# Kernel optimization log

Hardware: AMD Instinct MI355X
Metric: run time of the kernel (lower is better)

## Reference

```python
import jax, jax.numpy as jnp
import numpy as np

B, N, C = 2, 32768, 512
L, H = 64, 8
DH = C // H
NB = N // L
EG_HID = 16


def setup_inputs() -> dict:
    key = jax.random.key(0)
    ks = jax.random.split(key, 12)
    x = jax.random.normal(ks[0], (B, N, C), dtype=jnp.float32)
    attn_mask = jax.random.randint(ks[1], (NB, L, L), 0, 2, dtype=jnp.int32)
    edge_feats = jax.random.normal(ks[2], (NB, L, L, 4), dtype=jnp.float32)
    s = 1.0 / np.sqrt(C)
    w_qkv = jax.random.normal(ks[3], (C, 3 * C), dtype=jnp.float32) * s
    b_qkv = jnp.zeros((3 * C,), dtype=jnp.float32)
    w_proj = jax.random.normal(ks[4], (C, C), dtype=jnp.float32) * s
    b_proj = jnp.zeros((C,), dtype=jnp.float32)
    w_eg1 = jax.random.normal(ks[5], (4, EG_HID), dtype=jnp.float32) * 0.01
    b_eg1 = jnp.zeros((EG_HID,), dtype=jnp.float32)
    w_eg2 = jax.random.normal(ks[6], (EG_HID, H), dtype=jnp.float32) * 0.01
    b_eg2 = jnp.zeros((H,), dtype=jnp.float32)
    w_blk = jax.random.normal(ks[7], (C, H), dtype=jnp.float32) * 0.01
    b_blk = jnp.zeros((H,), dtype=jnp.float32)
    return {"x": x, "attn_mask": attn_mask, "edge_feats": edge_feats,
            "w_qkv": w_qkv, "b_qkv": b_qkv, "w_proj": w_proj, "b_proj": b_proj,
            "w_eg1": w_eg1, "b_eg1": b_eg1, "w_eg2": w_eg2, "b_eg2": b_eg2,
            "w_blk": w_blk, "b_blk": b_blk}


def reference(x, attn_mask, edge_feats, w_qkv, b_qkv, w_proj, b_proj,
              w_eg1, b_eg1, w_eg2, b_eg2, w_blk, b_blk):
    scale = DH ** -0.5
    x_blk = x.reshape(B, NB, L, C)
    # bias_physics: (B, NB, L, L, 4), expanded across batch
    bias = jnp.broadcast_to(edge_feats[None], (B, NB, L, L, 4))
    idx = jnp.arange(L)
    # zero diagonal, set channel 3 of diagonal to 1
    bias = bias.at[:, :, idx, idx, :].set(0.0)
    bias = bias.at[:, :, idx, idx, 3].set(1.0)
    # mask: (B, NB, L, L); ensure each query row attends to at least itself
    mask = jnp.broadcast_to(attn_mask[None], (B, NB, L, L))
    need_diag = (mask.sum(axis=-1) < 1).astype(mask.dtype)  # (B, NB, L)
    diag = mask[:, :, idx, idx]
    mask = mask.at[:, :, idx, idx].set(jnp.maximum(diag, need_diag))
    # qkv
    qkv = x_blk @ w_qkv + b_qkv  # (B, NB, L, 3C)
    q = qkv[..., :C].reshape(B, NB, L, H, DH)
    k = qkv[..., C:2 * C].reshape(B, NB, L, H, DH)
    v = qkv[..., 2 * C:].reshape(B, NB, L, H, DH)
    scores = jnp.einsum('bnqhd,bnkhd->bnqkh', q, k) * scale
    scores = scores + bias[..., 3:4]
    mask_e = (mask[..., None] == 0)  # (B, NB, L, L, 1)
    scores = jnp.where(mask_e, -jnp.inf, scores)
    attn_probs = jax.nn.softmax(scores, axis=3)
    # edge-gate MLP: 4 -> 16 (exact GELU) -> H
    gate = jax.nn.gelu(bias @ w_eg1 + b_eg1, approximate=False) @ w_eg2 + b_eg2
    gate = jnp.where(mask_e, 0.0, gate)
    combined = attn_probs + gate
    x_mid = jnp.einsum('bnqkh,bnkhd->bnqhd', combined, v)  # (B, NB, L, H, DH)
    # block route token
    block_node = x_blk.mean(axis=2, keepdims=True)  # (B, NB, 1, C)
    v_block = (block_node @ w_qkv + b_qkv)[..., 2 * C:].reshape(B, NB, 1, H, DH)
    g_block = jax.nn.sigmoid(x_blk @ w_blk + b_blk)  # (B, NB, L, H)
    x_mid = x_mid + g_block[..., None] * v_block
    out = x_mid.reshape(B, NB, L, C) @ w_proj + b_proj
    return out.reshape(B, N, C)
```

## Files before the change

kernel.cpp:

```cpp
#include <hip/hip_runtime.h>

typedef unsigned short u16;
typedef __attribute__((ext_vector_type(8))) short bf16x8;
typedef __attribute__((ext_vector_type(4))) float f32x4;

#define NTOK 32768
#define CC 512
#define HH 8
#define LL 64
#define NBLK 512

__device__ __forceinline__ u16 f2bf(float f) {
    unsigned int u = __float_as_uint(f);
    unsigned int r = u + 0x7fffu + ((u >> 16) & 1u);
    return (u16)(r >> 16);
}
__device__ __forceinline__ float bf2f(u16 h) {
    return __uint_as_float(((unsigned int)h) << 16);
}
__device__ __forceinline__ bf16x8 bc8(uint4 v) {
    return __builtin_bit_cast(bf16x8, v);
}
__device__ __forceinline__ void dma16(const u16* g, u16* l) {
    __builtin_amdgcn_global_load_lds((const __attribute__((address_space(1))) void*)g,
                                     (__attribute__((address_space(3))) void*)l, 16, 0, 0);
}

__global__ __launch_bounds__(256) void convert_gblock_kernel(const float* __restrict__ x,
                                                             u16* __restrict__ xbf,
                                                             const float* __restrict__ w_blk,
                                                             const float* __restrict__ b_blk,
                                                             float* __restrict__ gbl) {
    __shared__ float wbs[4608];
    int tid = threadIdx.x;
    for (int i = tid; i < 4096; i += 256) wbs[i + (i >> 6)] = w_blk[i];
    size_t tok = (size_t)blockIdx.x * 4 + (tid >> 6);
    int lane = tid & 63;
    int c0 = lane * 8;
    const float4* p = (const float4*)(x + tok * CC + c0);
    float4 a = p[0], b = p[1];
    uint4 o;
    o.x = (unsigned)f2bf(a.x) | ((unsigned)f2bf(a.y) << 16);
    o.y = (unsigned)f2bf(a.z) | ((unsigned)f2bf(a.w) << 16);
    o.z = (unsigned)f2bf(b.x) | ((unsigned)f2bf(b.y) << 16);
    o.w = (unsigned)f2bf(b.z) | ((unsigned)f2bf(b.w) << 16);
    *(uint4*)(xbf + tok * CC + c0) = o;
    float xv[8] = {a.x, a.y, a.z, a.w, b.x, b.y, b.z, b.w};
    __syncthreads();
    float acc[8];
#pragma unroll
    for (int h = 0; h < 8; ++h) acc[h] = 0.f;
#pragma unroll
    for (int j = 0; j < 8; ++j) {
        const float* wr = &wbs[(c0 + j) * 8 + lane];
#pragma unroll
        for (int h = 0; h < 8; ++h) acc[h] += xv[j] * wr[h];
    }
#pragma unroll
    for (int h = 0; h < 8; ++h) {
#pragma unroll
        for (int off = 1; off < 64; off <<= 1) acc[h] += __shfl_xor(acc[h], off);
    }
    float v = acc[0];
#pragma unroll
    for (int h = 1; h < 8; ++h) v = (lane == h) ? acc[h] : v;
    if (lane < 8) gbl[tok * 8 + lane] = 1.f / (1.f + __expf(-(v + b_blk[lane])));
}

__global__ __launch_bounds__(256) void transpose_bf16_kernel(const float* __restrict__ in,
                                                             u16* __restrict__ out,
                                                             int K, int Nn) {
    __shared__ float tile[32][33];
    int n0 = blockIdx.x * 32, k0 = blockIdx.y * 32;
    int tx = threadIdx.x & 31, ty = threadIdx.x >> 5;
#pragma unroll
    for (int i = 0; i < 4; ++i)
        tile[ty + i * 8][tx] = in[(size_t)(k0 + ty + i * 8) * Nn + n0 + tx];
    __syncthreads();
#pragma unroll
    for (int i = 0; i < 4; ++i)
        out[(size_t)(n0 + ty + i * 8) * K + k0 + tx] = f2bf(tile[tx][ty + i * 8]);
}

__global__ __launch_bounds__(256) void gate_sbias_kernel(const int* __restrict__ mask,
                                                         const float* __restrict__ edge,
                                                         const float* __restrict__ w1,
                                                         const float* __restrict__ b1,
                                                         const float* __restrict__ w2,
                                                         const float* __restrict__ b2,
                                                         u16* __restrict__ gate2,
                                                         u16* __restrict__ sbias2) {
    __shared__ float w1s[64], b1s[16], w2s[128], b2s[8];
    __shared__ int nds[64];
    int t = threadIdx.x;
    int nb = blockIdx.x;
    if (t < 64) w1s[t] = w1[t];
    if (t < 16) b1s[t] = b1[t];
    if (t < 128) w2s[t] = w2[t];
    if (t < 8) b2s[t] = b2[t];
    if (t < 64) {
        int s = 0;
        const int* mr = mask + (size_t)(nb * 64 + t) * 64;
#pragma unroll 8
        for (int k = 0; k < 64; ++k) s += mr[k];
        nds[t] = (s < 1) ? 1 : 0;
    }
    __syncthreads();
#pragma unroll 1
    for (int it = 0; it < 16; ++it) {
        int p = it * 256 + t;
        int q = p >> 6, k = p & 63;
        int pk = (k & 15) * 4 + (k >> 4);
        int mv = mask[(size_t)(nb * 64 + q) * 64 + k];
        float e0, e1, e2, e3;
        if (q == k) {
            mv = max(mv, nds[q]);
            e0 = e1 = e2 = 0.f;
            e3 = 1.f;
        } else {
            const float* ep = edge + ((size_t)(nb * 64 + q) * 64 + k) * 4;
            e0 = ep[0]; e1 = ep[1]; e2 = ep[2]; e3 = ep[3];
        }
        sbias2[(size_t)(nb * 64 + q) * 64 + pk] = f2bf(mv ? e3 : -1e30f);
        float g[8];
#pragma unroll
        for (int hh = 0; hh < 8; ++hh) g[hh] = b2s[hh];
#pragma unroll
        for (int j = 0; j < 16; ++j) {
            float hpre = e0 * w1s[j] + e1 * w1s[16 + j] + e2 * w1s[32 + j] + e3 * w1s[48 + j] + b1s[j];
            float hg = 0.5f * hpre * (1.f + erff(hpre * 0.70710678f));
#pragma unroll
            for (int hh = 0; hh < 8; ++hh) g[hh] += hg * w2s[j * 8 + hh];
        }
#pragma unroll
        for (int hh = 0; hh < 8; ++hh)
            gate2[(((size_t)nb * 8 + hh) * 64 + q) * 64 + pk] = f2bf(mv ? g[hh] : 0.f);
    }
}

__global__ __launch_bounds__(256) void qkv_gemm_kernel(const u16* __restrict__ xbf,
                                                       const u16* __restrict__ wqkvT,
                                                       const float* __restrict__ b_qkv,
                                                       u16* __restrict__ qkv) {
    __shared__ __align__(16) u16 As[128 * 64], Bs[128 * 64];
    int tid = threadIdx.x;
    int n0 = blockIdx.x * 128;
    int m0 = blockIdx.y * 128;
    int lane = tid & 63, l15 = lane & 15, quad = lane >> 4, wave = tid >> 6;
    int r8 = lane >> 3, jch = lane & 7;
    int js = jch ^ r8;
    int mwl = (wave >> 1) * 64, nwl = (wave & 1) * 64;
    int sw = l15 & 7;

    f32x4 acc[4][4];
#pragma unroll
    for (int i = 0; i < 4; ++i)
#pragma unroll
        for (int j = 0; j < 4; ++j) acc[i][j] = (f32x4){0.f, 0.f, 0.f, 0.f};

    int arow[4], brow[4];
#pragma unroll
    for (int i = 0; i < 4; ++i) arow[i] = (mwl + i * 16 + l15) * 64;
#pragma unroll
    for (int j = 0; j < 4; ++j) brow[j] = (nwl + j * 16 + l15) * 64;

    const u16* gA = xbf + (size_t)(m0 + wave * 32 + r8) * CC + js * 8;
    const u16* gB = wqkvT + (size_t)(n0 + wave * 32 + r8) * CC + js * 8;
    u16* lA = As + wave * 32 * 64;
    u16* lB = Bs + wave * 32 * 64;

    for (int kt = 0; kt < 8; ++kt) {
        int k0 = kt * 64;
#pragma unroll
        for (int t = 0; t < 4; ++t) {
            dma16(gA + (size_t)t * 8 * CC + k0, lA + t * 8 * 64);
            dma16(gB + (size_t)t * 8 * CC + k0, lB + t * 8 * 64);
        }
        __syncthreads();
#pragma unroll
        for (int kk = 0; kk < 2; ++kk) {
            int ch = ((kk * 4 + quad) ^ sw) * 8;
            bf16x8 a[4], bb[4];
#pragma unroll
            for (int i = 0; i < 4; ++i) a[i] = *(const bf16x8*)&As[arow[i] + ch];
#pragma unroll
            for (int j = 0; j < 4; ++j) bb[j] = *(const bf16x8*)&Bs[brow[j] + ch];
#pragma unroll
            for (int i = 0; i < 4; ++i)
#pragma unroll
                for (int j = 0; j < 4; ++j)
                    acc[i][j] = __builtin_amdgcn_mfma_f32_16x16x32_bf16(a[i], bb[j], acc[i][j], 0, 0, 0);
        }
        __syncthreads();
    }
#pragma unroll
    for (int i = 0; i < 4; ++i)
#pragma unroll
        for (int j = 0; j < 4; ++j) {
            int col = n0 + nwl + j * 16 + l15;
            float bp = b_qkv[col];
#pragma unroll
            for (int r = 0; r < 4; ++r) {
                int row = m0 + mwl + i * 16 + quad * 4 + r;
                qkv[(size_t)row * 1536 + col] = f2bf(acc[i][j][r] + bp);
            }
        }
}

__global__ __launch_bounds__(256) void outproj_kernel(const u16* __restrict__ xmid,
                                                      const u16* __restrict__ wprojT,
                                                      const float* __restrict__ b_proj,
                                                      float* __restrict__ out) {
    __shared__ __align__(16) u16 As[128 * 64], Bs[128 * 64];
    int tid = threadIdx.x;
    int n0 = blockIdx.x * 128;
    int m0 = blockIdx.y * 128;
    int lane = tid & 63, l15 = lane & 15, quad = lane >> 4, wave = tid >> 6;
    int r8 = lane >> 3, jch = lane & 7;
    int js = jch ^ r8;
    int mwl = (wave >> 1) * 64, nwl = (wave & 1) * 64;
    int sw = l15 & 7;

    f32x4 acc[4][4];
#pragma unroll
    for (int i = 0; i < 4; ++i)
#pragma unroll
        for (int j = 0; j < 4; ++j) acc[i][j] = (f32x4){0.f, 0.f, 0.f, 0.f};

    int arow[4], brow[4];
#pragma unroll
    for (int i = 0; i < 4; ++i) arow[i] = (mwl + i * 16 + l15) * 64;
#pragma unroll
    for (int j = 0; j < 4; ++j) brow[j] = (nwl + j * 16 + l15) * 64;

    const u16* gA = xmid + (size_t)(m0 + wave * 32 + r8) * CC + js * 8;
    const u16* gB = wprojT + (size_t)(n0 + wave * 32 + r8) * CC + js * 8;
    u16* lA = As + wave * 32 * 64;
    u16* lB = Bs + wave * 32 * 64;

    for (int kt = 0; kt < 8; ++kt) {
        int k0 = kt * 64;
#pragma unroll
        for (int t = 0; t < 4; ++t) {
            dma16(gA + (size_t)t * 8 * CC + k0, lA + t * 8 * 64);
            dma16(gB + (size_t)t * 8 * CC + k0, lB + t * 8 * 64);
        }
        __syncthreads();
#pragma unroll
        for (int kk = 0; kk < 2; ++kk) {
            int ch = ((kk * 4 + quad) ^ sw) * 8;
            bf16x8 a[4], bb[4];
#pragma unroll
            for (int i = 0; i < 4; ++i) a[i] = *(const bf16x8*)&As[arow[i] + ch];
#pragma unroll
            for (int j = 0; j < 4; ++j) bb[j] = *(const bf16x8*)&Bs[brow[j] + ch];
#pragma unroll
            for (int i = 0; i < 4; ++i)
#pragma unroll
                for (int j = 0; j < 4; ++j)
                    acc[i][j] = __builtin_amdgcn_mfma_f32_16x16x32_bf16(a[i], bb[j], acc[i][j], 0, 0, 0);
        }
        __syncthreads();
    }
#pragma unroll
    for (int i = 0; i < 4; ++i)
#pragma unroll
        for (int j = 0; j < 4; ++j) {
            int col = n0 + nwl + j * 16 + l15;
            float bp = b_proj[col];
#pragma unroll
            for (int r = 0; r < 4; ++r) {
                int row = m0 + mwl + i * 16 + quad * 4 + r;
                out[(size_t)row * CC + col] = acc[i][j][r] + bp;
            }
        }
}

__global__ __launch_bounds__(256) void attn_kernel(const u16* __restrict__ qkv,
                                                   const u16* __restrict__ sbias2,
                                                   const u16* __restrict__ gate2,
                                                   const float* __restrict__ gbl,
                                                   u16* __restrict__ xmid) {
    __shared__ u16 VT[64 * 72], Ps[64 * 72];
    __shared__ float gl[64], vbl[64];
    int tid = threadIdx.x;
    int bid = blockIdx.x;
    int h = bid & 7, nb = (bid >> 3) & 511, b = bid >> 12;
    int lane = tid & 63, l15 = lane & 15, quad = lane >> 4, wave = tid >> 6;
    int m0 = wave * 16;
    size_t blockrow = (size_t)(b * NTOK + nb * 64);
    const u16* qbase = qkv + blockrow * 1536 + h * 64;

    {
        int key = tid & 63, d0 = (tid >> 6) * 16;
        const uint4* vsrc = (const uint4*)(qbase + (size_t)key * 1536 + 1024 + d0);
        uint4 v0 = vsrc[0], v1 = vsrc[1];
        u16 tmp[16];
        *(uint4*)tmp = v0;
        *(uint4*)(tmp + 8) = v1;
#pragma unroll
        for (int j = 0; j < 16; ++j) VT[(d0 + j) * 72 + key] = tmp[j];
    }
    if (tid < 64) gl[tid] = gbl[(blockrow + tid) * 8 + h];
    __syncthreads();

    if (tid < 64) {
        float s = 0.f;
#pragma unroll 8
        for (int k = 0; k < 64; ++k) s += bf2f(VT[tid * 72 + k]);
        vbl[tid] = s * 0.015625f;
    }

    f32x4 sc[4];
#pragma unroll
    for (int t = 0; t < 4; ++t) sc[t] = (f32x4){0.f, 0.f, 0.f, 0.f};
#pragma unroll
    for (int kk = 0; kk < 2; ++kk) {
        bf16x8 a = bc8(*(const uint4*)(qbase + (size_t)(m0 + l15) * 1536 + kk * 32 + quad * 8));
#pragma unroll
        for (int t = 0; t < 4; ++t) {
            bf16x8 bb = bc8(*(const uint4*)(qbase + (size_t)(t * 16 + l15) * 1536 + 512 + kk * 32 + quad * 8));
            sc[t] = __builtin_amdgcn_mfma_f32_16x16x32_bf16(a, bb, sc[t], 0, 0, 0);
        }
    }
    {
        const u16* sb2 = sbias2 + (size_t)nb * 4096;
        const u16* gp2 = gate2 + ((size_t)nb * 8 + h) * 4096;
#pragma unroll
        for (int r = 0; r < 4; ++r) {
            int q = m0 + quad * 4 + r;
            ushort4 sv = *(const ushort4*)(sb2 + (q * 16 + l15) * 4);
            float bias_t[4] = {bf2f(sv.x), bf2f(sv.y), bf2f(sv.z), bf2f(sv.w)};
            float mx = -3e38f;
#pragma unroll
            for (int t = 0; t < 4; ++t) {
                float v = sc[t][r] * 0.125f + bias_t[t];
                sc[t][r] = v;
                mx = fmaxf(mx, v);
            }
            mx = fmaxf(mx, __shfl_xor(mx, 1));
            mx = fmaxf(mx, __shfl_xor(mx, 2));
            mx = fmaxf(mx, __shfl_xor(mx, 4));
            mx = fmaxf(mx, __shfl_xor(mx, 8));
            float sum = 0.f;
#pragma unroll
            for (int t = 0; t < 4; ++t) {
                float p = __expf(sc[t][r] - mx);
                sc[t][r] = p;
                sum += p;
            }
            sum += __shfl_xor(sum, 1);
            sum += __shfl_xor(sum, 2);
            sum += __shfl_xor(sum, 4);
            sum += __shfl_xor(sum, 8);
            float inv = 1.f / sum;
            ushort4 gv = *(const ushort4*)(gp2 + (q * 16 + l15) * 4);
            float gate_t[4] = {bf2f(gv.x), bf2f(gv.y), bf2f(gv.z), bf2f(gv.w)};
#pragma unroll
            for (int t = 0; t < 4; ++t) {
                float comb = sc[t][r] * inv + gate_t[t];
                Ps[q * 72 + t * 16 + l15] = f2bf(comb);
            }
        }
    }
    __syncthreads();

    f32x4 o[4];
#pragma unroll
    for (int t = 0; t < 4; ++t) o[t] = (f32x4){0.f, 0.f, 0.f, 0.f};
#pragma unroll
    for (int kk = 0; kk < 2; ++kk) {
        bf16x8 a = *(const bf16x8*)&Ps[(m0 + l15) * 72 + kk * 32 + quad * 8];
#pragma unroll
        for (int t = 0; t < 4; ++t) {
            bf16x8 bb = *(const bf16x8*)&VT[(t * 16 + l15) * 72 + kk * 32 + quad * 8];
            o[t] = __builtin_amdgcn_mfma_f32_16x16x32_bf16(a, bb, o[t], 0, 0, 0);
        }
    }
#pragma unroll
    for (int t = 0; t < 4; ++t) {
#pragma unroll
        for (int r = 0; r < 4; ++r) {
            int q = m0 + quad * 4 + r, d = t * 16 + l15;
            float v = o[t][r] + gl[q] * vbl[d];
            xmid[(blockrow + q) * CC + h * 64 + d] = f2bf(v);
        }
    }
}

extern "C" void kernel_launch(void* const* d_in, const int* in_sizes, int n_in,
                              void* d_out, int out_size, void* d_ws, size_t ws_size,
                              hipStream_t stream) {
    const float* x = (const float*)d_in[0];
    const int* attn_mask = (const int*)d_in[1];
    const float* edge = (const float*)d_in[2];
    const float* w_qkv = (const float*)d_in[3];
    const float* b_qkv = (const float*)d_in[4];
    const float* w_proj = (const float*)d_in[5];
    const float* b_proj = (const float*)d_in[6];
    const float* w_eg1 = (const float*)d_in[7];
    const float* b_eg1 = (const float*)d_in[8];
    const float* w_eg2 = (const float*)d_in[9];
    const float* b_eg2 = (const float*)d_in[10];
    const float* w_blk = (const float*)d_in[11];
    const float* b_blk = (const float*)d_in[12];
    float* out = (float*)d_out;

    char* ws = (char*)d_ws;
    u16* xbf = (u16*)ws;
    u16* xmid = (u16*)ws;
    u16* qkv = (u16*)(ws + 67108864);
    u16* gate2 = (u16*)(ws + 268435456);
    u16* sbias2 = (u16*)(ws + 301989888);
    u16* wqkvT = (u16*)(ws + 306184192);
    u16* wprojT = (u16*)(ws + 307757056);
    float* gbl = (float*)(ws + 308281344);

    convert_gblock_kernel<<<16384, 256, 0, stream>>>(x, xbf, w_blk, b_blk, gbl);
    transpose_bf16_kernel<<<dim3(48, 16), 256, 0, stream>>>(w_qkv, wqkvT, 512, 1536);
    transpose_bf16_kernel<<<dim3(16, 16), 256, 0, stream>>>(w_proj, wprojT, 512, 512);
    gate_sbias_kernel<<<512, 256, 0, stream>>>(attn_mask, edge, w_eg1, b_eg1, w_eg2, b_eg2,
                                               gate2, sbias2);
    qkv_gemm_kernel<<<dim3(12, 512), 256, 0, stream>>>(xbf, wqkvT, b_qkv, qkv);
    attn_kernel<<<8192, 256, 0, stream>>>(qkv, sbias2, gate2, gbl, xmid);
    outproj_kernel<<<dim3(4, 512), 256, 0, stream>>>(xmid, wprojT, b_proj, out);
}
```

Before: 718.0 us.

## Store QKV head-planar, remap GEMM blocks per XCD, split gate kernel

The QKV GEMM now writes its output in a head-planar layout (plane of 64 columns × all tokens), so the attention kernel reads contiguous 128-byte rows for Q, K and V instead of rows strided by 1536 elements. Both GEMMs use a flat 1D grid with a block-index remap that groups consecutive logical tiles onto the same XCD (stride 8), to improve L2 reuse of the A and B tiles. The gate/sbias kernel is split four ways over query rows to raise parallelism. The planar store scatters writes at 64-element granularity, which may cost some write efficiency in the GEMM epilogue.

```diff
diff --git a/kernel.cpp b/kernel.cpp
--- a/kernel.cpp
+++ b/kernel.cpp
@@ -9,6 +9,7 @@
 #define HH 8
 #define LL 64
 #define NBLK 512
+#define MTOK 65536
 
 __device__ __forceinline__ u16 f2bf(float f) {
     unsigned int u = __float_as_uint(f);
@@ -91,30 +92,33 @@
                                                          u16* __restrict__ gate2,
                                                          u16* __restrict__ sbias2) {
     __shared__ float w1s[64], b1s[16], w2s[128], b2s[8];
-    __shared__ int nds[64];
+    __shared__ int nds[16];
     int t = threadIdx.x;
-    int nb = blockIdx.x;
+    int nb = blockIdx.x >> 2;
+    int qt = blockIdx.x & 3;
     if (t < 64) w1s[t] = w1[t];
     if (t < 16) b1s[t] = b1[t];
     if (t < 128) w2s[t] = w2[t];
     if (t < 8) b2s[t] = b2[t];
-    if (t < 64) {
+    if (t >= 128 && t < 144) {
+        int q = qt * 16 + (t - 128);
         int s = 0;
-        const int* mr = mask + (size_t)(nb * 64 + t) * 64;
+        const int* mr = mask + (size_t)(nb * 64 + q) * 64;
 #pragma unroll 8
         for (int k = 0; k < 64; ++k) s += mr[k];
-        nds[t] = (s < 1) ? 1 : 0;
+        nds[t - 128] = (s < 1) ? 1 : 0;
     }
     __syncthreads();
 #pragma unroll 1
-    for (int it = 0; it < 16; ++it) {
+    for (int it = 0; it < 4; ++it) {
         int p = it * 256 + t;
-        int q = p >> 6, k = p & 63;
+        int ql = p >> 6, k = p & 63;
+        int q = qt * 16 + ql;
         int pk = (k & 15) * 4 + (k >> 4);
         int mv = mask[(size_t)(nb * 64 + q) * 64 + k];
         float e0, e1, e2, e3;
         if (q == k) {
-            mv = max(mv, nds[q]);
+            mv = max(mv, nds[ql]);
             e0 = e1 = e2 = 0.f;
             e3 = 1.f;
         } else {
@@ -144,8 +148,10 @@
                                                        u16* __restrict__ qkv) {
     __shared__ __align__(16) u16 As[128 * 64], Bs[128 * 64];
     int tid = threadIdx.x;
-    int n0 = blockIdx.x * 128;
-    int m0 = blockIdx.y * 128;
+    int flat = blockIdx.x;
+    int logical = (flat & 7) * 768 + (flat >> 3);
+    int n0 = (logical % 12) * 128;
+    int m0 = (logical / 12) * 128;
     int lane = tid & 63, l15 = lane & 15, quad = lane >> 4, wave = tid >> 6;
     int r8 = lane >> 3, jch = lane & 7;
     int js = jch ^ r8;
@@ -198,11 +204,13 @@
 #pragma unroll
         for (int j = 0; j < 4; ++j) {
             int col = n0 + nwl + j * 16 + l15;
+            int plane = col >> 6;
+            int d = col & 63;
             float bp = b_qkv[col];
 #pragma unroll
             for (int r = 0; r < 4; ++r) {
                 int row = m0 + mwl + i * 16 + quad * 4 + r;
-                qkv[(size_t)row * 1536 + col] = f2bf(acc[i][j][r] + bp);
+                qkv[((size_t)plane * MTOK + row) * 64 + d] = f2bf(acc[i][j][r] + bp);
             }
         }
 }
@@ -213,8 +221,10 @@
                                                       float* __restrict__ out) {
     __shared__ __align__(16) u16 As[128 * 64], Bs[128 * 64];
     int tid = threadIdx.x;
-    int n0 = blockIdx.x * 128;
-    int m0 = blockIdx.y * 128;
+    int flat = blockIdx.x;
+    int logical = (flat & 7) * 256 + (flat >> 3);
+    int n0 = (logical & 3) * 128;
+    int m0 = (logical >> 2) * 128;
     int lane = tid & 63, l15 = lane & 15, quad = lane >> 4, wave = tid >> 6;
     int r8 = lane >> 3, jch = lane & 7;
     int js = jch ^ r8;
@@ -289,11 +299,13 @@
     int lane = tid & 63, l15 = lane & 15, quad = lane >> 4, wave = tid >> 6;
     int m0 = wave * 16;
     size_t blockrow = (size_t)(b * NTOK + nb * 64);
-    const u16* qbase = qkv + blockrow * 1536 + h * 64;
+    const u16* qq = qkv + ((size_t)h * MTOK + blockrow) * 64;
+    const u16* qk = qq + (size_t)8 * MTOK * 64;
+    const u16* qv = qq + (size_t)16 * MTOK * 64;
 
     {
         int key = tid & 63, d0 = (tid >> 6) * 16;
-        const uint4* vsrc = (const uint4*)(qbase + (size_t)key * 1536 + 1024 + d0);
+        const uint4* vsrc = (const uint4*)(qv + (size_t)key * 64 + d0);
         uint4 v0 = vsrc[0], v1 = vsrc[1];
         u16 tmp[16];
         *(uint4*)tmp = v0;
@@ -316,10 +328,10 @@
     for (int t = 0; t < 4; ++t) sc[t] = (f32x4){0.f, 0.f, 0.f, 0.f};
 #pragma unroll
     for (int kk = 0; kk < 2; ++kk) {
-        bf16x8 a = bc8(*(const uint4*)(qbase + (size_t)(m0 + l15) * 1536 + kk * 32 + quad * 8));
+        bf16x8 a = bc8(*(const uint4*)(qq + (size_t)(m0 + l15) * 64 + kk * 32 + quad * 8));
 #pragma unroll
         for (int t = 0; t < 4; ++t) {
-            bf16x8 bb = bc8(*(const uint4*)(qbase + (size_t)(t * 16 + l15) * 1536 + 512 + kk * 32 + quad * 8));
+            bf16x8 bb = bc8(*(const uint4*)(qk + (size_t)(t * 16 + l15) * 64 + kk * 32 + quad * 8));
             sc[t] = __builtin_amdgcn_mfma_f32_16x16x32_bf16(a, bb, sc[t], 0, 0, 0);
         }
     }
@@ -419,9 +431,9 @@
     convert_gblock_kernel<<<16384, 256, 0, stream>>>(x, xbf, w_blk, b_blk, gbl);
     transpose_bf16_kernel<<<dim3(48, 16), 256, 0, stream>>>(w_qkv, wqkvT, 512, 1536);
     transpose_bf16_kernel<<<dim3(16, 16), 256, 0, stream>>>(w_proj, wprojT, 512, 512);
-    gate_sbias_kernel<<<512, 256, 0, stream>>>(attn_mask, edge, w_eg1, b_eg1, w_eg2, b_eg2,
-                                               gate2, sbias2);
-    qkv_gemm_kernel<<<dim3(12, 512), 256, 0, stream>>>(xbf, wqkvT, b_qkv, qkv);
+    gate_sbias_kernel<<<2048, 256, 0, stream>>>(attn_mask, edge, w_eg1, b_eg1, w_eg2, b_eg2,
+                                                gate2, sbias2);
+    qkv_gemm_kernel<<<6144, 256, 0, stream>>>(xbf, wqkvT, b_qkv, qkv);
     attn_kernel<<<8192, 256, 0, stream>>>(qkv, sbias2, gate2, gbl, xmid);
-    outproj_kernel<<<dim3(4, 512), 256, 0, stream>>>(xmid, wprojT, b_proj, out);
-}
+    outproj_kernel<<<2048, 256, 0, stream>>>(xmid, wprojT, b_proj, out);
+}
```

After: 700.3 us. 1.03x faster.
